# Optimization experiments

Hardware: AMD Instinct MI355X
Metric: run time of the kernel (lower is better)

## Reference

```python
import jax, jax.numpy as jnp
import numpy as np

B, T, D, H = 2, 2048, 1024, 16
DH = D // H
THETA = 10000.0
MAX_SEQ_LEN = 2048


def setup_inputs() -> dict:
    key = jax.random.key(0)
    kx, kqkv, ko = jax.random.split(key, 3)
    # trunc_normal init matching the torch Linear (std=sqrt(2/(fan_in+fan_out)), clipped at 3 sigma)
    sigma_qkv = (2.0 / (D + 3 * D)) ** 0.5
    sigma_o = (2.0 / (D + D)) ** 0.5
    W_qkv = jax.random.truncated_normal(kqkv, -3.0, 3.0, (3 * D, D), jnp.float32) * sigma_qkv
    W_o = jax.random.truncated_normal(ko, -3.0, 3.0, (D, D), jnp.float32) * sigma_o
    # RoPE caches: angles[t, i] = t / theta^(2i/d_k)
    dims = jnp.arange(0, DH, 2, dtype=jnp.float32)
    inv_freq = 1.0 / (THETA ** (dims / DH))  # [DH/2]
    angles = jnp.arange(MAX_SEQ_LEN, dtype=jnp.float32)[:, None] * inv_freq[None, :]  # [T, DH/2]
    return {
        "x": jax.random.normal(kx, (B, T, D), jnp.float32),
        "token_positions": jnp.arange(T, dtype=jnp.int64 if jax.config.jax_enable_x64 else jnp.int32),
        "W_qkv": W_qkv,
        "W_o": W_o,
        "cos_cached": jnp.cos(angles),
        "sin_cached": jnp.sin(angles),
    }


def _apply_rope(x, cos, sin):
    # x: [b, h, t, dh]; cos/sin: [t, dh/2] broadcast over (b, h)
    x1 = x[..., 0::2]
    x2 = x[..., 1::2]
    r1 = x1 * cos - x2 * sin
    r2 = x1 * sin + x2 * cos
    # interleave back: (.., dh/2, 2) -> (.., dh)
    return jnp.stack([r1, r2], axis=-1).reshape(x.shape)


def reference(x, token_positions, W_qkv, W_o, cos_cached, sin_cached):
    b, t, d = x.shape
    qkv = jnp.einsum("btd,ed->bte", x, W_qkv)  # [b, t, 3d]
    q, k, v = jnp.split(qkv, 3, axis=-1)

    def to_heads(z):
        return z.reshape(b, t, H, DH).transpose(0, 2, 1, 3)  # [b, h, t, dh]

    q, k, v = to_heads(q), to_heads(k), to_heads(v)

    cos = cos_cached[token_positions]  # [t, dh/2]
    sin = sin_cached[token_positions]
    q = _apply_rope(q, cos, sin)
    k = _apply_rope(k, cos, sin)

    scale = 1.0 / jnp.sqrt(jnp.asarray(DH, x.dtype))
    scores = jnp.einsum("bhqd,bhkd->bhqk", q, k) * scale  # full TxT (naive, matches source)
    causal = jnp.tril(jnp.ones((t, t), dtype=bool))  # [t, t]
    scores = jnp.where(causal[None, None, :, :], scores, -jnp.inf)
    attn = jax.nn.softmax(scores, axis=-1)
    out = jnp.einsum("bhqk,bhkd->bhqd", attn, v)  # [b, h, t, dh]
    out = out.transpose(0, 2, 1, 3).reshape(b, t, d)
    return jnp.einsum("btd,ed->bte", out, W_o)
```

## Files before the change

### kernel.cpp

```cpp
#include <hip/hip_runtime.h>
#include <hip/hip_bf16.h>
#include <stdint.h>

#define Bn  2
#define Tn  2048
#define Dn  1024
#define Hn  16
#define DHn 64
#define QSCALE 0.1803368801111204f

typedef unsigned short u16;
typedef __attribute__((ext_vector_type(8))) short s16x8;
typedef __attribute__((ext_vector_type(8))) unsigned short u16x8;
typedef __attribute__((ext_vector_type(4))) unsigned short u16x4;
typedef __attribute__((ext_vector_type(4))) float f32x4;

#define MFMA(a, b, c) __builtin_amdgcn_mfma_f32_16x16x32_bf16((a), (b), (c), 0, 0, 0)

__device__ __forceinline__ u16 f2bf(float f) {
  union { __hip_bfloat16 b; u16 u; } c;
  c.b = __float2bfloat16(f);
  return c.u;
}
__device__ __forceinline__ float bf2f(u16 u) {
  union { u16 u; __hip_bfloat16 b; } c;
  c.u = u;
  return __bfloat162float(c.b);
}

__device__ __forceinline__ void lds16(void* lds, const void* g) {
  __builtin_amdgcn_global_load_lds((__attribute__((address_space(1))) void*)(g),
                                   (__attribute__((address_space(3))) void*)(lds), 16, 0, 0);
}

__global__ __launch_bounds__(256) void k_cvt2(const float* __restrict__ s0, int n0,
                                              const float* __restrict__ s1, int n1,
                                              u16* __restrict__ dst) {
  int i = blockIdx.x * blockDim.x + threadIdx.x;
  const int stride = gridDim.x * blockDim.x;
  const int nt = n0 + n1;
  for (; i < nt; i += stride) {
    float4 v = (i < n0) ? ((const float4*)s0)[i] : ((const float4*)s1)[i - n0];
    u16x4 o;
    o[0] = f2bf(v.x); o[1] = f2bf(v.y); o[2] = f2bf(v.z); o[3] = f2bf(v.w);
    ((u16x4*)dst)[i] = o;
  }
}

__global__ __launch_bounds__(256) void k_cvt(const float* __restrict__ src,
                                             u16* __restrict__ dst, int n4) {
  int i = blockIdx.x * blockDim.x + threadIdx.x;
  const int stride = gridDim.x * blockDim.x;
  for (; i < n4; i += stride) {
    float4 v = ((const float4*)src)[i];
    u16x4 o;
    o[0] = f2bf(v.x); o[1] = f2bf(v.y); o[2] = f2bf(v.z); o[3] = f2bf(v.w);
    ((u16x4*)dst)[i] = o;
  }
}

__global__ __launch_bounds__(256) void k_qkv(
    const u16* __restrict__ xb, const u16* __restrict__ wb,
    const int* __restrict__ tokpos,
    const float* __restrict__ cosc, const float* __restrict__ sinc,
    u16* __restrict__ qb, u16* __restrict__ kb, u16* __restrict__ vtb)
{
  __shared__ u16 smem[17408];
  const int tid  = threadIdx.x;
  const int bcol = blockIdx.x;
  const int brow = blockIdx.y;
  const int lane = tid & 63, w = tid >> 6;
  const int wr = w >> 1, wc = w & 1;
  const int l15 = lane & 15, l4 = lane >> 4;
  const int lrow = lane >> 2;
  const int gsw  = (((lane & 3) ^ ((lrow >> 1) & 3)) * 8);
  const int rsw  = (l15 >> 1) & 3;

  const u16* xrow = xb + (size_t)(brow * 128) * 1024;
  const u16* wrow = wb + (size_t)(bcol * 128) * 1024;

  f32x4 acc[4][4] = {};

  {
    const int r0 = w * 32;
    lds16(&smem[r0 * 32],              xrow + (size_t)(r0 + lrow) * 1024 + gsw);
    lds16(&smem[(r0 + 16) * 32],       xrow + (size_t)(r0 + 16 + lrow) * 1024 + gsw);
    lds16(&smem[8192 + r0 * 32],       wrow + (size_t)(r0 + lrow) * 1024 + gsw);
    lds16(&smem[8192 + (r0 + 16) * 32],wrow + (size_t)(r0 + 16 + lrow) * 1024 + gsw);
  }

  for (int kt = 0; kt < 32; ++kt) {
    const int cur = kt & 1;
    const u16* Asb = smem + cur * 4096;
    const u16* Bsb = smem + 8192 + cur * 4096;
    if (kt < 31) {
      u16* Asn = smem + (cur ^ 1) * 4096;
      u16* Bsn = smem + 8192 + (cur ^ 1) * 4096;
      const int k1 = (kt + 1) * 32;
      const int r0 = w * 32;
      lds16(&Asn[r0 * 32],        xrow + (size_t)(r0 + lrow) * 1024 + k1 + gsw);
      lds16(&Asn[(r0 + 16) * 32], xrow + (size_t)(r0 + 16 + lrow) * 1024 + k1 + gsw);
      lds16(&Bsn[r0 * 32],        wrow + (size_t)(r0 + lrow) * 1024 + k1 + gsw);
      lds16(&Bsn[(r0 + 16) * 32], wrow + (size_t)(r0 + 16 + lrow) * 1024 + k1 + gsw);
      asm volatile("s_waitcnt vmcnt(4)" ::: "memory");
    } else {
      asm volatile("s_waitcnt vmcnt(0)" ::: "memory");
    }
    __builtin_amdgcn_s_barrier();
    __builtin_amdgcn_sched_barrier(0);
    __builtin_amdgcn_s_setprio(1);
    {
      const int gr = (l4 ^ rsw) * 8;
      s16x8 af[4], bf[4];
#pragma unroll
      for (int m = 0; m < 4; ++m)
        af[m] = *(const s16x8*)&Asb[(wr * 64 + m * 16 + l15) * 32 + gr];
#pragma unroll
      for (int n = 0; n < 4; ++n)
        bf[n] = *(const s16x8*)&Bsb[(wc * 64 + n * 16 + l15) * 32 + gr];
#pragma unroll
      for (int m = 0; m < 4; ++m)
#pragma unroll
        for (int n = 0; n < 4; ++n)
          acc[m][n] = MFMA(af[m], bf[n], acc[m][n]);
    }
    __builtin_amdgcn_s_setprio(0);
    __builtin_amdgcn_sched_barrier(0);
    __builtin_amdgcn_s_barrier();
  }

#pragma unroll
  for (int m = 0; m < 4; ++m)
#pragma unroll
    for (int n = 0; n < 4; ++n)
#pragma unroll
      for (int r = 0; r < 4; ++r)
        smem[(wr * 64 + m * 16 + l4 * 4 + r) * 136 + wc * 64 + n * 16 + l15] =
            f2bf(acc[m][n][r]);
  __syncthreads();

  if (bcol < 16) {
    u16* dst; float sc;
    if (bcol < 8) { dst = qb; sc = QSCALE; } else { dst = kb; sc = 1.0f; }
#pragma unroll
    for (int ph = 0; ph < 8; ++ph) {
      const int task = ph * 256 + tid;
      const int lr   = task >> 4;
      const int cg   = task & 15;
      const int rowg = brow * 128 + lr;
      const int b = rowg >> 11, t = rowg & 2047;
      const int rem = (bcol * 128 + cg * 8) & 1023;
      const int h = rem >> 6, dh0 = rem & 63;
      u16x8 v = *(const u16x8*)&smem[lr * 136 + cg * 8];
      const int pos = tokpos[t];
      const float4 cv = *(const float4*)&cosc[pos * 32 + (dh0 >> 1)];
      const float4 sv = *(const float4*)&sinc[pos * 32 + (dh0 >> 1)];
      const float cc[4] = {cv.x, cv.y, cv.z, cv.w};
      const float ss[4] = {sv.x, sv.y, sv.z, sv.w};
      u16x8 o;
#pragma unroll
      for (int p = 0; p < 4; ++p) {
        const float x1 = bf2f(v[2 * p]), x2 = bf2f(v[2 * p + 1]);
        o[2 * p]     = f2bf((x1 * cc[p] - x2 * ss[p]) * sc);
        o[2 * p + 1] = f2bf((x1 * ss[p] + x2 * cc[p]) * sc);
      }
      *(u16x8*)(dst + ((size_t)(b * Hn + h) * Tn + t) * DHn + dh0) = o;
    }
  } else {
    const int b  = (brow * 128) >> 11;
    const int t0 = (brow * 128) & 2047;
#pragma unroll
    for (int ph = 0; ph < 8; ++ph) {
      const int task = ph * 256 + tid;
      const int col = task & 127;
      const int tg  = task >> 7;
      const int h  = 2 * (bcol - 16) + (col >> 6);
      const int dh = col & 63;
      u16x8 v;
#pragma unroll
      for (int j = 0; j < 8; ++j) v[j] = smem[(tg * 8 + j) * 136 + col];
      *(u16x8*)(vtb + ((size_t)(b * Hn + h) * DHn + dh) * Tn + t0 + tg * 8) = v;
    }
  }
}

__global__ __launch_bounds__(256) void k_attn(
    const u16* __restrict__ qbuf, const u16* __restrict__ kbuf,
    const u16* __restrict__ vtb, u16* __restrict__ ob)
{
  __shared__ u16 Ks[2][64][64];
  __shared__ u16 Vs[2][64][64];
  __shared__ u16 Ps[4][16][64];

  const int tid  = threadIdx.x;
  const int lane = tid & 63, w = tid >> 6;
  const int l15 = lane & 15, l4 = lane >> 4;
  const int lrow = lane >> 3;
  const int gsw  = ((lane & 7) ^ (lane >> 3)) * 8;
  const int rsw  = l15 & 7;

  const int lin = blockIdx.x;
  const int bh  = lin & 31;
  const int a   = (lin >> 5) & 7, rb = lin >> 8;
  const int qblk = (rb == 0) ? a : (rb == 1) ? (15 - a) : (rb == 2) ? (16 + a) : (31 - a);
  const int b = bh >> 4, h = bh & 15;

  const u16* Qh = qbuf + (size_t)bh * Tn * DHn;
  const u16* Kh = kbuf + (size_t)bh * Tn * DHn;
  const u16* Vh = vtb  + (size_t)bh * DHn * Tn;

  const int q0 = qblk * 64 + w * 16;
  const int ntiles = qblk + 1;

  const s16x8 qf0 = *(const s16x8*)(Qh + (size_t)(q0 + l15) * 64 + l4 * 8);
  const s16x8 qf1 = *(const s16x8*)(Qh + (size_t)(q0 + l15) * 64 + 32 + l4 * 8);

  const s16x8 onesv = {(short)0x3F80, (short)0x3F80, (short)0x3F80, (short)0x3F80,
                       (short)0x3F80, (short)0x3F80, (short)0x3F80, (short)0x3F80};

  f32x4 o[4] = {};
  f32x4 o5 = {};
  float m = -3.0e38f;

  {
    const int r0 = w * 16;
    lds16(&Ks[0][r0][0],     Kh + (size_t)(r0 + lrow) * 64 + gsw);
    lds16(&Ks[0][r0 + 8][0], Kh + (size_t)(r0 + 8 + lrow) * 64 + gsw);
    lds16(&Vs[0][r0][0],     Vh + (size_t)(r0 + lrow) * Tn + gsw);
    lds16(&Vs[0][r0 + 8][0], Vh + (size_t)(r0 + 8 + lrow) * Tn + gsw);
  }

  for (int it = 0; it < ntiles; ++it) {
    const int buf = it & 1;
    if (it + 1 < ntiles) {
      const int nb = buf ^ 1;
      const int kv1 = (it + 1) * 64;
      const int r0 = w * 16;
      lds16(&Ks[nb][r0][0],     Kh + (size_t)(kv1 + r0 + lrow) * 64 + gsw);
      lds16(&Ks[nb][r0 + 8][0], Kh + (size_t)(kv1 + r0 + 8 + lrow) * 64 + gsw);
      lds16(&Vs[nb][r0][0],     Vh + (size_t)(r0 + lrow) * Tn + kv1 + gsw);
      lds16(&Vs[nb][r0 + 8][0], Vh + (size_t)(r0 + 8 + lrow) * Tn + kv1 + gsw);
      asm volatile("s_waitcnt vmcnt(4)" ::: "memory");
    } else {
      asm volatile("s_waitcnt vmcnt(0)" ::: "memory");
    }
    __builtin_amdgcn_s_barrier();
    __builtin_amdgcn_sched_barrier(0);

    f32x4 s[4] = {};
    __builtin_amdgcn_s_setprio(1);
#pragma unroll
    for (int ks = 0; ks < 2; ++ks) {
      const s16x8 qf = ks ? qf1 : qf0;
      const int gr = ((ks * 4 + l4) ^ rsw) * 8;
#pragma unroll
      for (int hh = 0; hh < 4; ++hh) {
        const s16x8 kf = *(const s16x8*)&Ks[buf][hh * 16 + l15][gr];
        s[hh] = MFMA(kf, qf, s[hh]);
      }
    }
    __builtin_amdgcn_s_setprio(0);

    if (it == ntiles - 1) {
      const int kvb = it * 64 + l4 * 4;
      const int qg  = q0 + l15;
#pragma unroll
      for (int hh = 0; hh < 4; ++hh)
#pragma unroll
        for (int rr = 0; rr < 4; ++rr)
          if (kvb + hh * 16 + rr > qg) s[hh][rr] = -3.0e38f;
    }

    const float a0 = fmaxf(fmaxf(s[0][0], s[0][1]), s[0][2]);
    const float a1 = fmaxf(fmaxf(s[0][3], s[1][0]), s[1][1]);
    const float a2 = fmaxf(fmaxf(s[1][2], s[1][3]), s[2][0]);
    const float a3 = fmaxf(fmaxf(s[2][1], s[2][2]), s[2][3]);
    const float a4 = fmaxf(fmaxf(s[3][0], s[3][1]), s[3][2]);
    float tmax = fmaxf(fmaxf(fmaxf(a0, a1), fmaxf(a2, a3)), fmaxf(a4, s[3][3]));
    tmax = fmaxf(tmax, __shfl_xor(tmax, 16));
    tmax = fmaxf(tmax, __shfl_xor(tmax, 32));

    if (__any(tmax > m + 8.0f)) {
      const float mn    = fmaxf(m, tmax);
      const float alpha = __builtin_amdgcn_exp2f(m - mn);
      m = mn;
#pragma unroll
      for (int n = 0; n < 4; ++n)
#pragma unroll
        for (int rr = 0; rr < 4; ++rr) o[n][rr] *= alpha;
#pragma unroll
      for (int rr = 0; rr < 4; ++rr) o5[rr] *= alpha;
    }

#pragma unroll
    for (int hh = 0; hh < 4; ++hh) {
      u16x4 pk;
#pragma unroll
      for (int rr = 0; rr < 4; ++rr)
        pk[rr] = f2bf(__builtin_amdgcn_exp2f(s[hh][rr] - m));
      const int pg = ((hh << 1) + (l4 >> 1)) ^ rsw;
      *(u16x4*)&Ps[w][l15][pg * 8 + (l4 & 1) * 4] = pk;
    }

    const s16x8 pf0 = *(const s16x8*)&Ps[w][l15][(l4 ^ rsw) * 8];
    const s16x8 pf1 = *(const s16x8*)&Ps[w][l15][((4 + l4) ^ rsw) * 8];

    __builtin_amdgcn_s_setprio(1);
#pragma unroll
    for (int n = 0; n < 4; ++n) {
      const int g0 = (l4 ^ rsw) * 8, g1 = ((4 + l4) ^ rsw) * 8;
      const s16x8 vf0 = *(const s16x8*)&Vs[buf][n * 16 + l15][g0];
      const s16x8 vf1 = *(const s16x8*)&Vs[buf][n * 16 + l15][g1];
      o[n] = MFMA(vf0, pf0, o[n]);
      o[n] = MFMA(vf1, pf1, o[n]);
    }
    o5 = MFMA(onesv, pf0, o5);
    o5 = MFMA(onesv, pf1, o5);
    __builtin_amdgcn_s_setprio(0);
    __builtin_amdgcn_sched_barrier(0);
    __builtin_amdgcn_s_barrier();
  }

  const float inv = 1.0f / o5[0];
  const int t = q0 + l15;
#pragma unroll
  for (int n = 0; n < 4; ++n) {
    u16x4 ov;
#pragma unroll
    for (int rr = 0; rr < 4; ++rr) ov[rr] = f2bf(o[n][rr] * inv);
    *(u16x4*)(ob + (size_t)(b * Tn + t) * Dn + h * 64 + n * 16 + l4 * 4) = ov;
  }
}

__global__ __launch_bounds__(256) void k_out(
    const u16* __restrict__ ob, const u16* __restrict__ wob,
    float* __restrict__ out)
{
  __shared__ u16 smem[24576];
  const int tid  = threadIdx.x;
  const int bcol = blockIdx.x;
  const int brow = blockIdx.y;
  const int lane = tid & 63, w = tid >> 6;
  const int wr = w >> 1, wc = w & 1;
  const int l15 = lane & 15, l4 = lane >> 4;
  const int lrow = lane >> 3;
  const int gsw  = ((lane & 7) ^ (lane >> 3)) * 8;
  const int rsw  = l15 & 7;

  f32x4 acc[4][2] = {};

#pragma unroll
  for (int c = 0; c < 4; ++c) {
    const int r0 = w * 32 + c * 8;
    lds16(&smem[r0 * 64], ob + (size_t)(brow * 128 + r0 + lrow) * 1024 + gsw);
  }
#pragma unroll
  for (int c = 0; c < 2; ++c) {
    const int r0 = w * 16 + c * 8;
    lds16(&smem[16384 + r0 * 64], wob + (size_t)(bcol * 64 + r0 + lrow) * 1024 + gsw);
  }

  for (int kt = 0; kt < 16; ++kt) {
    const int cur = kt & 1;
    const u16* Asb = smem + cur * 8192;
    const u16* Bsb = smem + 16384 + cur * 4096;
    if (kt < 15) {
      u16* Asn = smem + (cur ^ 1) * 8192;
      u16* Bsn = smem + 16384 + (cur ^ 1) * 4096;
      const int k1 = (kt + 1) * 64;
#pragma unroll
      for (int c = 0; c < 4; ++c) {
        const int r0 = w * 32 + c * 8;
        lds16(&Asn[r0 * 64], ob + (size_t)(brow * 128 + r0 + lrow) * 1024 + k1 + gsw);
      }
#pragma unroll
      for (int c = 0; c < 2; ++c) {
        const int r0 = w * 16 + c * 8;
        lds16(&Bsn[r0 * 64], wob + (size_t)(bcol * 64 + r0 + lrow) * 1024 + k1 + gsw);
      }
      asm volatile("s_waitcnt vmcnt(6)" ::: "memory");
    } else {
      asm volatile("s_waitcnt vmcnt(0)" ::: "memory");
    }
    __builtin_amdgcn_s_barrier();
    __builtin_amdgcn_sched_barrier(0);
    __builtin_amdgcn_s_setprio(1);
#pragma unroll
    for (int kk = 0; kk < 64; kk += 32) {
      const int gc = (kk >> 3) + l4;
      s16x8 af[4], bf[2];
#pragma unroll
      for (int m = 0; m < 4; ++m)
        af[m] = *(const s16x8*)&Asb[(wr * 64 + m * 16 + l15) * 64 + ((gc ^ rsw) * 8)];
#pragma unroll
      for (int n = 0; n < 2; ++n)
        bf[n] = *(const s16x8*)&Bsb[(wc * 32 + n * 16 + l15) * 64 + ((gc ^ rsw) * 8)];
#pragma unroll
      for (int m = 0; m < 4; ++m)
#pragma unroll
        for (int n = 0; n < 2; ++n)
          acc[m][n] = MFMA(af[m], bf[n], acc[m][n]);
    }
    __builtin_amdgcn_s_setprio(0);
    __builtin_amdgcn_sched_barrier(0);
    __builtin_amdgcn_s_barrier();
  }

#pragma unroll
  for (int m = 0; m < 4; ++m) {
    const int rowb = brow * 128 + wr * 64 + m * 16 + l4 * 4;
#pragma unroll
    for (int n = 0; n < 2; ++n) {
      const int colg = bcol * 64 + wc * 32 + n * 16 + l15;
#pragma unroll
      for (int r = 0; r < 4; ++r)
        out[(size_t)(rowb + r) * 1024 + colg] = acc[m][n][r];
    }
  }
}

extern "C" void kernel_launch(void* const* d_in, const int* in_sizes, int n_in,
                              void* d_out, int out_size, void* d_ws, size_t ws_size,
                              hipStream_t stream) {
  const float* x      = (const float*)d_in[0];
  const int*   tokpos = (const int*)d_in[1];
  const float* wqkv   = (const float*)d_in[2];
  const float* wo     = (const float*)d_in[3];
  const float* cosc   = (const float*)d_in[4];
  const float* sinc   = (const float*)d_in[5];
  float* out = (float*)d_out;

  u16* xb    = (u16*)d_ws;
  u16* wqkvb = xb + (size_t)Bn * Tn * Dn;
  u16* qb    = wqkvb + (size_t)3 * Dn * Dn;
  u16* kb    = qb + (size_t)Bn * Tn * Dn;
  u16* vtb   = kb + (size_t)Bn * Tn * Dn;
  u16* ob    = xb;
  u16* wob   = wqkvb;

  dim3 blk(256);
  k_cvt2<<<dim3(2048), blk, 0, stream>>>(x, (Bn * Tn * Dn) / 4,
                                         wqkv, (3 * Dn * Dn) / 4, xb);

  k_qkv<<<dim3(24, 32), blk, 0, stream>>>(xb, wqkvb, tokpos, cosc, sinc, qb, kb, vtb);

  k_cvt<<<dim3(1024), blk, 0, stream>>>(wo, wob, (Dn * Dn) / 4);

  k_attn<<<dim3(1024), blk, 0, stream>>>(qb, kb, vtb, ob);

  k_out<<<dim3(16, 32), blk, 0, stream>>>(ob, wob, out);
}
```

Measured before the change: 107.2 us.

## Load K/V fragments directly from global into registers, drop LDS staging

The attention kernel no longer stages K and V tiles through double-buffered shared memory with async loads and barriers. Each wave now reads its MFMA fragments for K and V directly from global memory at the start of each iteration. This removes LDS writes and reads and the per-iteration workgroup barriers. In exchange, all four waves reread the same K/V tile from cache, the explicit prefetch of the next tile is lost, and register pressure rises.

```diff
diff --git a/kernel.cpp b/kernel.cpp
--- a/kernel.cpp
+++ b/kernel.cpp
@@ -188,15 +188,11 @@
     const u16* __restrict__ qbuf, const u16* __restrict__ kbuf,
     const u16* __restrict__ vtb, u16* __restrict__ ob)
 {
-  __shared__ u16 Ks[2][64][64];
-  __shared__ u16 Vs[2][64][64];
   __shared__ u16 Ps[4][16][64];
 
   const int tid  = threadIdx.x;
   const int lane = tid & 63, w = tid >> 6;
   const int l15 = lane & 15, l4 = lane >> 4;
-  const int lrow = lane >> 3;
-  const int gsw  = ((lane & 7) ^ (lane >> 3)) * 8;
   const int rsw  = l15 & 7;
 
   const int lin = blockIdx.x;
@@ -218,51 +214,41 @@
   const s16x8 onesv = {(short)0x3F80, (short)0x3F80, (short)0x3F80, (short)0x3F80,
                        (short)0x3F80, (short)0x3F80, (short)0x3F80, (short)0x3F80};
 
+  const u16* kp0 = Kh + (size_t)(l15) * 64 + l4 * 8;
+  const u16* vp0 = Vh + (size_t)(l15) * Tn + l4 * 8;
+
   f32x4 o[4] = {};
   f32x4 o5 = {};
   float m = -3.0e38f;
 
-  {
-    const int r0 = w * 16;
-    lds16(&Ks[0][r0][0],     Kh + (size_t)(r0 + lrow) * 64 + gsw);
-    lds16(&Ks[0][r0 + 8][0], Kh + (size_t)(r0 + 8 + lrow) * 64 + gsw);
-    lds16(&Vs[0][r0][0],     Vh + (size_t)(r0 + lrow) * Tn + gsw);
-    lds16(&Vs[0][r0 + 8][0], Vh + (size_t)(r0 + 8 + lrow) * Tn + gsw);
-  }
-
   for (int it = 0; it < ntiles; ++it) {
-    const int buf = it & 1;
-    if (it + 1 < ntiles) {
-      const int nb = buf ^ 1;
-      const int kv1 = (it + 1) * 64;
-      const int r0 = w * 16;
-      lds16(&Ks[nb][r0][0],     Kh + (size_t)(kv1 + r0 + lrow) * 64 + gsw);
-      lds16(&Ks[nb][r0 + 8][0], Kh + (size_t)(kv1 + r0 + 8 + lrow) * 64 + gsw);
-      lds16(&Vs[nb][r0][0],     Vh + (size_t)(r0 + lrow) * Tn + kv1 + gsw);
-      lds16(&Vs[nb][r0 + 8][0], Vh + (size_t)(r0 + 8 + lrow) * Tn + kv1 + gsw);
-      asm volatile("s_waitcnt vmcnt(4)" ::: "memory");
-    } else {
-      asm volatile("s_waitcnt vmcnt(0)" ::: "memory");
-    }
-    __builtin_amdgcn_s_barrier();
-    __builtin_amdgcn_sched_barrier(0);
+    const int kv0 = it * 64;
+
+    s16x8 kf[2][4], vf[2][4];
+#pragma unroll
+    for (int ks = 0; ks < 2; ++ks)
+#pragma unroll
+      for (int n = 0; n < 4; ++n)
+        vf[ks][n] = *(const s16x8*)(vp0 + (size_t)(n * 16) * Tn + kv0 + ks * 32);
+#pragma unroll
+    for (int ks = 0; ks < 2; ++ks)
+#pragma unroll
+      for (int hh = 0; hh < 4; ++hh)
+        kf[ks][hh] = *(const s16x8*)(kp0 + (size_t)(kv0 + hh * 16) * 64 + ks * 32);
 
     f32x4 s[4] = {};
     __builtin_amdgcn_s_setprio(1);
 #pragma unroll
     for (int ks = 0; ks < 2; ++ks) {
       const s16x8 qf = ks ? qf1 : qf0;
-      const int gr = ((ks * 4 + l4) ^ rsw) * 8;
-#pragma unroll
-      for (int hh = 0; hh < 4; ++hh) {
-        const s16x8 kf = *(const s16x8*)&Ks[buf][hh * 16 + l15][gr];
-        s[hh] = MFMA(kf, qf, s[hh]);
-      }
+#pragma unroll
+      for (int hh = 0; hh < 4; ++hh)
+        s[hh] = MFMA(kf[ks][hh], qf, s[hh]);
     }
     __builtin_amdgcn_s_setprio(0);
 
     if (it == ntiles - 1) {
-      const int kvb = it * 64 + l4 * 4;
+      const int kvb = kv0 + l4 * 4;
       const int qg  = q0 + l15;
 #pragma unroll
       for (int hh = 0; hh < 4; ++hh)
@@ -308,17 +294,12 @@
     __builtin_amdgcn_s_setprio(1);
 #pragma unroll
     for (int n = 0; n < 4; ++n) {
-      const int g0 = (l4 ^ rsw) * 8, g1 = ((4 + l4) ^ rsw) * 8;
-      const s16x8 vf0 = *(const s16x8*)&Vs[buf][n * 16 + l15][g0];
-      const s16x8 vf1 = *(const s16x8*)&Vs[buf][n * 16 + l15][g1];
-      o[n] = MFMA(vf0, pf0, o[n]);
-      o[n] = MFMA(vf1, pf1, o[n]);
+      o[n] = MFMA(vf[0][n], pf0, o[n]);
+      o[n] = MFMA(vf[1][n], pf1, o[n]);
     }
     o5 = MFMA(onesv, pf0, o5);
     o5 = MFMA(onesv, pf1, o5);
     __builtin_amdgcn_s_setprio(0);
-    __builtin_amdgcn_sched_barrier(0);
-    __builtin_amdgcn_s_barrier();
   }
 
   const float inv = 1.0f / o5[0];
```

New measurement: 181.6 us. 69.4% more time.
